# Performance work log

Measured on AMD Instinct MI355X. Metric: run time of the kernel, lower is better.

The kernel has to match this reference:

```python
import jax, jax.numpy as jnp
import numpy as np

EMBED_DIM = 768
NUM_HEADS = 12
HEAD_DIM = EMBED_DIM // NUM_HEADS
MLP_HIDDEN = int(EMBED_DIM * 4.0)
LN_EPS = 1e-5


def setup_inputs() -> dict:
    key = jax.random.key(0)
    ks = jax.random.split(key, 8)
    C, H = EMBED_DIM, MLP_HIDDEN
    s = 0.02
    return {
        "x": jax.random.normal(ks[0], (2, 2048, C), dtype=jnp.float32),
        "ln1_g": jnp.ones((C,), jnp.float32),
        "ln1_b": jnp.zeros((C,), jnp.float32),
        "qkv_w": jax.random.normal(ks[1], (3 * C, C), jnp.float32) * s,
        "proj_w": jax.random.normal(ks[2], (C, C), jnp.float32) * s,
        "proj_b": jnp.zeros((C,), jnp.float32),
        "ln2_g": jnp.ones((C,), jnp.float32),
        "ln2_b": jnp.zeros((C,), jnp.float32),
        "fc1_w": jax.random.normal(ks[3], (H, C), jnp.float32) * s,
        "fc1_b": jnp.zeros((H,), jnp.float32),
        "fc2_w": jax.random.normal(ks[4], (C, H), jnp.float32) * s,
        "fc2_b": jnp.zeros((C,), jnp.float32),
    }


def _layernorm(x, g, b):
    mu = jnp.mean(x, axis=-1, keepdims=True)
    var = jnp.mean(jnp.square(x - mu), axis=-1, keepdims=True)
    return (x - mu) * jax.lax.rsqrt(var + LN_EPS) * g + b


def reference(x, ln1_g, ln1_b, qkv_w, proj_w, proj_b, ln2_g, ln2_b,
              fc1_w, fc1_b, fc2_w, fc2_b):
    B, N, C = x.shape
    Hh, Dh = NUM_HEADS, HEAD_DIM
    scale = Dh ** -0.5

    # --- attention branch (pre-norm) ---
    h = _layernorm(x, ln1_g, ln1_b)
    qkv = h @ qkv_w.T                                   # [B,N,3C]
    qkv = qkv.reshape(B, N, 3, Hh, Dh)
    q = qkv[:, :, 0].transpose(0, 2, 1, 3)              # [B,H,N,D]
    k = qkv[:, :, 1].transpose(0, 2, 1, 3)
    v = qkv[:, :, 2].transpose(0, 2, 1, 3)
    attn = jnp.einsum('bhnd,bhmd->bhnm', q, k) * scale  # [B,H,N,N]
    attn = jax.nn.softmax(attn, axis=-1)
    o = jnp.einsum('bhnm,bhmd->bhnd', attn, v)          # [B,H,N,D]
    o = o.transpose(0, 2, 1, 3).reshape(B, N, C)
    x = x + o @ proj_w.T + proj_b

    # --- MLP branch (pre-norm), exact GELU like nn.GELU ---
    h = _layernorm(x, ln2_g, ln2_b)
    h = jax.nn.gelu(h @ fc1_w.T + fc1_b, approximate=False)
    x = x + h @ fc2_w.T + fc2_b
    return x
```

## Files before the change

kernel.cpp:

```cpp
#include <hip/hip_runtime.h>
#include <hip/hip_bf16.h>
#include <cstdint>
#include <math.h>


typedef __bf16 bf16_t;
typedef bf16_t bf16x4 __attribute__((ext_vector_type(4)));
typedef bf16_t bf16x8 __attribute__((ext_vector_type(8)));
typedef float floatx4 __attribute__((ext_vector_type(4)));

#define AS1 __attribute__((address_space(1)))
#define AS3 __attribute__((address_space(3)))

__device__ __forceinline__ void async_load16(const void* g, void* l) {
  const AS1 unsigned int* gp =
      reinterpret_cast<const AS1 unsigned int*>(reinterpret_cast<uintptr_t>(g));
  AS3 unsigned int* lp = reinterpret_cast<AS3 unsigned int*>(
      static_cast<unsigned int>(reinterpret_cast<uintptr_t>(l)));
  __builtin_amdgcn_global_load_lds(gp, lp, 16, 0, 0);
}

__device__ __forceinline__ bf16x8 lds_read8(const bf16_t* p) {
  return *reinterpret_cast<const bf16x8*>(p);
}

__global__ __launch_bounds__(256) void cvt_k(const float* __restrict__ in,
                                             bf16_t* __restrict__ out, int n4) {
  const int i = blockIdx.x * 256 + threadIdx.x;
  if (i < n4) {
    const float4 v = reinterpret_cast<const float4*>(in)[i];
    bf16x4 o;
    o[0] = (bf16_t)v.x; o[1] = (bf16_t)v.y; o[2] = (bf16_t)v.z; o[3] = (bf16_t)v.w;
    reinterpret_cast<bf16x4*>(out)[i] = o;
  }
}

__global__ __launch_bounds__(256) void cvt_all_k(
    const float* __restrict__ s0, const float* __restrict__ s1,
    const float* __restrict__ s2, const float* __restrict__ s3,
    bf16_t* __restrict__ d0, bf16_t* __restrict__ d1, bf16_t* __restrict__ d2,
    bf16_t* __restrict__ d3) {
  int i = blockIdx.x * 256 + threadIdx.x;
  const float* src;
  bf16_t* dst;
  if (i < 442368) { src = s0; dst = d0; }
  else if (i < 589824) { src = s1; dst = d1; i -= 442368; }
  else if (i < 1179648) { src = s2; dst = d2; i -= 589824; }
  else if (i < 1769472) { src = s3; dst = d3; i -= 1179648; }
  else return;
  const float4 v = reinterpret_cast<const float4*>(src)[i];
  bf16x4 o;
  o[0] = (bf16_t)v.x; o[1] = (bf16_t)v.y; o[2] = (bf16_t)v.z; o[3] = (bf16_t)v.w;
  reinterpret_cast<bf16x4*>(dst)[i] = o;
}

template <int INIT>
__global__ __launch_bounds__(256) void ln_k(const float* __restrict__ x,
                                            const float* __restrict__ g,
                                            const float* __restrict__ b,
                                            bf16_t* __restrict__ out,
                                            const float* __restrict__ b2,
                                            float* __restrict__ oinit) {
  const int row = blockIdx.x;
  const int tid = threadIdx.x;
  const float* xr = x + (long)row * 768;
  float v[3];
#pragma unroll
  for (int e = 0; e < 3; e++) v[e] = xr[tid + e * 256];
  float s = v[0] + v[1] + v[2];
  float ss = v[0] * v[0] + v[1] * v[1] + v[2] * v[2];
#pragma unroll
  for (int off = 32; off >= 1; off >>= 1) {
    s += __shfl_down(s, off, 64);
    ss += __shfl_down(ss, off, 64);
  }
  __shared__ float red[8];
  __shared__ float stat[2];
  const int wv = tid >> 6;
  if ((tid & 63) == 0) { red[wv] = s; red[4 + wv] = ss; }
  __syncthreads();
  if (tid == 0) {
    float S = red[0] + red[1] + red[2] + red[3];
    float SS = red[4] + red[5] + red[6] + red[7];
    float mu = S * (1.0f / 768.0f);
    float var = SS * (1.0f / 768.0f) - mu * mu;
    stat[0] = mu;
    stat[1] = rsqrtf(var + 1e-5f);
  }
  __syncthreads();
  const float mu = stat[0], rs = stat[1];
#pragma unroll
  for (int e = 0; e < 3; e++) {
    int c = tid + e * 256;
    out[(long)row * 768 + c] = (bf16_t)((v[e] - mu) * rs * g[c] + b[c]);
    if constexpr (INIT == 1) oinit[(long)row * 768 + c] = v[e] + b2[c];
  }
}

template <int MODE>
__global__ __launch_bounds__(256, 2) void gemm_k(
    const bf16_t* __restrict__ A, const bf16_t* __restrict__ Bt, int lda,
    int ldb, int keff, int Nld, const float* __restrict__ bias,
    bf16_t* __restrict__ out_bf, bf16_t* __restrict__ q_out,
    bf16_t* __restrict__ k_out, bf16_t* __restrict__ vt_out,
    const float* __restrict__ resid_f, float* __restrict__ out_f) {
  constexpr int BK = 32;
  __shared__ __align__(16) bf16_t As[3][128 * BK];
  __shared__ __align__(16) bf16_t Bs[3][128 * BK];

  const int tid = threadIdx.x;
  const int w = tid >> 6;
  const int lane = tid & 63;
  const int quad = lane >> 4;
  const int lid = lane & 15;
  const int wr = (w >> 1) * 64;
  const int wc = (w & 1) * 64;
  const int mBase = blockIdx.x * 128;
  const int nBase = blockIdx.y * 128;
  const int kOff = blockIdx.z * keff;

  const int ldsRowSub = lane >> 2;
  const int kblk = (lane & 3) ^ (ldsRowSub & 3) ^ ((ldsRowSub >> 2) & 3);
  const int rq0 = (quad ^ (lid & 3) ^ ((lid >> 2) & 3)) * 8;
  const int c0 = w * 2, c1 = w * 2 + 1;
  const int rowA0 = c0 * 16 + ldsRowSub, rowA1 = c1 * 16 + ldsRowSub;

  const bf16_t* Ag = A + (long)mBase * lda + kOff;
  const bf16_t* Bg = Bt + (long)nBase * ldb + kOff;

  floatx4 acc[4][4];
#pragma unroll
  for (int i = 0; i < 4; i++)
#pragma unroll
    for (int j = 0; j < 4; j++) acc[i][j] = (floatx4){0.f, 0.f, 0.f, 0.f};

  auto stage = [&](int b, int k0) {
    async_load16(Ag + (long)rowA0 * lda + k0 + kblk * 8, &As[b][c0 * 512]);
    async_load16(Ag + (long)rowA1 * lda + k0 + kblk * 8, &As[b][c1 * 512]);
    async_load16(Bg + (long)rowA0 * ldb + k0 + kblk * 8, &Bs[b][c0 * 512]);
    async_load16(Bg + (long)rowA1 * ldb + k0 + kblk * 8, &Bs[b][c1 * 512]);
  };

  const int iters = keff / BK;
  stage(0, 0);
  stage(1, BK);

  int cur = 0;
  for (int it = 0; it < iters; it++) {
    if (it + 1 < iters)
      asm volatile("s_waitcnt vmcnt(4) lgkmcnt(0)" ::: "memory");
    else
      asm volatile("s_waitcnt vmcnt(0) lgkmcnt(0)" ::: "memory");
    __builtin_amdgcn_s_barrier();
    if (it + 2 < iters) {
      int nb = cur + 2; if (nb >= 3) nb -= 3;
      stage(nb, (it + 2) * BK);
    }

    bf16x8 af[4], bfv[4];
#pragma unroll
    for (int i = 0; i < 4; i++)
      af[i] = lds_read8(&As[cur][(wr + i * 16 + lid) * BK + rq0]);
#pragma unroll
    for (int j = 0; j < 4; j++)
      bfv[j] = lds_read8(&Bs[cur][(wc + j * 16 + lid) * BK + rq0]);
#pragma unroll
    for (int i = 0; i < 4; i++)
#pragma unroll
      for (int j = 0; j < 4; j++)
        acc[i][j] = __builtin_amdgcn_mfma_f32_16x16x32_bf16(af[i], bfv[j],
                                                            acc[i][j], 0, 0, 0);
    cur = (cur == 2) ? 0 : cur + 1;
  }

#pragma unroll
  for (int i = 0; i < 4; i++) {
    const int mRow = mBase + wr + i * 16 + quad * 4;
#pragma unroll
    for (int j = 0; j < 4; j++) {
      const int n = nBase + wc + j * 16 + lid;
      if constexpr (MODE == 0) {
        const int which = n / 768;
        const int rem = n - which * 768;
        const int head = rem >> 6;
        const int d = rem & 63;
        const int b = mRow >> 11;
        const int t = mRow & 2047;
        const int bh = b * 12 + head;
        if (which == 2) {
          bf16x4 pk;
#pragma unroll
          for (int r = 0; r < 4; r++) pk[r] = (bf16_t)acc[i][j][r];
          const long off = ((long)bh * 64 + d) * 2048 + t;
          *reinterpret_cast<bf16x4*>(&vt_out[off]) = pk;
        } else if (which == 0) {
#pragma unroll
          for (int r = 0; r < 4; r++)
            q_out[((long)bh * 2048 + t + r) * 64 + d] =
                (bf16_t)(acc[i][j][r] * (0.125f * 1.44269504f));
        } else {
#pragma unroll
          for (int r = 0; r < 4; r++)
            k_out[((long)bh * 2048 + t + r) * 64 + d] = (bf16_t)acc[i][j][r];
        }
      } else if constexpr (MODE == 2) {
        const float bv = bias[n];
#pragma unroll
        for (int r = 0; r < 4; r++) {
          float v = acc[i][j][r] + bv;
          float ge = 0.5f * v * (1.0f + erff(v * 0.70710678118654752f));
          out_bf[(long)(mRow + r) * Nld + n] = (bf16_t)ge;
        }
      } else if constexpr (MODE == 3) {
        const float bv = bias[n];
#pragma unroll
        for (int r = 0; r < 4; r++) {
          const long off = (long)(mRow + r) * Nld + n;
          out_f[off] = resid_f[off] + acc[i][j][r] + bv;
        }
      } else {
#pragma unroll
        for (int r = 0; r < 4; r++) {
          const long off = (long)(mRow + r) * Nld + n;
          unsafeAtomicAdd(&out_f[off], acc[i][j][r]);
        }
      }
    }
  }
}

__global__ __launch_bounds__(512, 1) void flash_k(const bf16_t* __restrict__ q,
                                                  const bf16_t* __restrict__ kk,
                                                  const bf16_t* __restrict__ vt,
                                                  bf16_t* __restrict__ U,
                                                  float* __restrict__ lbuf) {
  constexpr int SK = 64, D = 64;
  __shared__ __align__(16) bf16_t Ks[3][SK * D];
  __shared__ __align__(16) bf16_t Vs[3][D * SK];

  const int tid = threadIdx.x;
  const int w = tid >> 6;
  const int lane = tid & 63;
  const int quad = lane >> 4;
  const int lid = lane & 15;
  const int bh = blockIdx.y;
  const int half = blockIdx.z;
  const int qBase = blockIdx.x * 128;

  const bf16_t* qg = q + ((long)bh * 2048 + qBase) * D;
  const bf16_t* kg = kk + ((long)bh * 2048 + half * 1024) * D;
  const bf16_t* vg = vt + (long)bh * D * 2048 + half * 1024;

  bf16x8 aq[2];
#pragma unroll
  for (int k2 = 0; k2 < 2; k2++)
    aq[k2] = *reinterpret_cast<const bf16x8*>(qg + (w * 16 + lid) * D +
                                              k2 * 32 + quad * 8);

  const int srow = lane >> 3;
  const int sdb = (lane & 7) ^ srow;
  const int rsw = lid & 7;

  auto stagef = [&](int b, int kc) {
    async_load16(kg + (long)(kc + w * 8 + srow) * D + sdb * 8, &Ks[b][w * 512]);
    async_load16(vg + (long)(w * 8 + srow) * 2048 + kc + sdb * 8, &Vs[b][w * 512]);
  };

  stagef(0, 0);
  stagef(1, 64);

  float lsum = 0.f;
  floatx4 oacc[4];
#pragma unroll
  for (int jo = 0; jo < 4; jo++) oacc[jo] = (floatx4){0.f, 0.f, 0.f, 0.f};

  int cur = 0;
  for (int kci = 0; kci < 16; kci++) {
    if (kci + 1 < 16)
      asm volatile("s_waitcnt vmcnt(2) lgkmcnt(0)" ::: "memory");
    else
      asm volatile("s_waitcnt vmcnt(0) lgkmcnt(0)" ::: "memory");
    __builtin_amdgcn_s_barrier();
    if (kci + 2 < 16) {
      int nb = cur + 2; if (nb >= 3) nb -= 3;
      stagef(nb, (kci + 2) * 64);
    }

    floatx4 sacc[4];
#pragma unroll
    for (int jm = 0; jm < 4; jm++) sacc[jm] = (floatx4){0.f, 0.f, 0.f, 0.f};
    __builtin_amdgcn_s_setprio(1);
#pragma unroll
    for (int k2 = 0; k2 < 2; k2++) {
#pragma unroll
      for (int jm = 0; jm < 4; jm++) {
        const bf16x8 ak = lds_read8(
            &Ks[cur][(jm * 16 + lid) * D + (((k2 * 4 + quad) ^ rsw) * 8)]);
        sacc[jm] =
            __builtin_amdgcn_mfma_f32_16x16x32_bf16(ak, aq[k2], sacc[jm], 0, 0, 0);
      }
    }
    __builtin_amdgcn_s_setprio(0);

    bf16x8 ap[2];
#pragma unroll
    for (int k2 = 0; k2 < 2; k2++) {
      uint32_t pk[2][2];
#pragma unroll
      for (int j = 0; j < 2; j++) {
        const int jm = k2 * 2 + j;
        const float p0 = exp2f(sacc[jm][0]);
        const float p1 = exp2f(sacc[jm][1]);
        const float p2 = exp2f(sacc[jm][2]);
        const float p3 = exp2f(sacc[jm][3]);
        lsum += ((p0 + p1) + p2) + p3;
        asm("v_cvt_pk_bf16_f32 %0, %1, %2" : "=v"(pk[j][0]) : "v"(p0), "v"(p1));
        asm("v_cvt_pk_bf16_f32 %0, %1, %2" : "=v"(pk[j][1]) : "v"(p2), "v"(p3));
      }
      asm("v_permlane32_swap_b32 %0, %1" : "+v"(pk[0][0]), "+v"(pk[1][0]));
      asm("v_permlane16_swap_b32 %0, %1" : "+v"(pk[0][0]), "+v"(pk[1][0]));
      asm("v_permlane32_swap_b32 %0, %1" : "+v"(pk[0][1]), "+v"(pk[1][1]));
      asm("v_permlane16_swap_b32 %0, %1" : "+v"(pk[0][1]), "+v"(pk[1][1]));
      union { uint32_t u[4]; bf16x8 v; } au;
      au.u[0] = pk[0][0];
      au.u[1] = pk[0][1];
      au.u[2] = pk[1][0];
      au.u[3] = pk[1][1];
      ap[k2] = au.v;
    }

    __builtin_amdgcn_s_setprio(1);
#pragma unroll
    for (int k2 = 0; k2 < 2; k2++) {
#pragma unroll
      for (int jo = 0; jo < 4; jo++) {
        const bf16x8 bv = lds_read8(
            &Vs[cur][(jo * 16 + lid) * SK + (((k2 * 4 + quad) ^ rsw) * 8)]);
        oacc[jo] =
            __builtin_amdgcn_mfma_f32_16x16x32_bf16(ap[k2], bv, oacc[jo], 0, 0, 0);
      }
    }
    __builtin_amdgcn_s_setprio(0);
    cur = (cur == 2) ? 0 : cur + 1;
  }

  lsum += __shfl_xor(lsum, 16, 64);
  lsum += __shfl_xor(lsum, 32, 64);

  const long lrow = ((long)half * 24 + bh) * 2048 + qBase + w * 16;
  if (quad == 0) lbuf[lrow + lid] = lsum;

  bf16_t* Ub = U + (((long)half * 24 + bh) * 2048 + qBase) * D;
#pragma unroll
  for (int jo = 0; jo < 4; jo++) {
#pragma unroll
    for (int r = 0; r < 4; r++) {
      const int t = w * 16 + quad * 4 + r;
      Ub[(long)t * D + jo * 16 + lid] = (bf16_t)oacc[jo][r];
    }
  }
}

__global__ __launch_bounds__(256) void combine_k(const bf16_t* __restrict__ U,
                                                 const float* __restrict__ lbuf,
                                                 bf16_t* __restrict__ o) {
  const int idx = blockIdx.x * 256 + threadIdx.x;
  const int bh = idx >> 17;
  const int rem = idx & 131071;
  const int t = rem >> 6;
  const int d = rem & 63;
  const float l0 = lbuf[bh * 2048 + t];
  const float l1 = lbuf[(24 + bh) * 2048 + t];
  const float u = (float)U[idx] + (float)U[3145728 + idx];
  const int b = bh / 12;
  const int head = bh - b * 12;
  o[((long)b * 2048 + t) * 768 + head * 64 + d] = (bf16_t)(u / (l0 + l1));
}

extern "C" void kernel_launch(void* const* d_in, const int* in_sizes, int n_in,
                              void* d_out, int out_size, void* d_ws,
                              size_t ws_size, hipStream_t stream) {
  (void)in_sizes; (void)n_in; (void)out_size;
  const float* x = (const float*)d_in[0];
  const float* ln1_g = (const float*)d_in[1];
  const float* ln1_b = (const float*)d_in[2];
  const float* qkv_w = (const float*)d_in[3];
  const float* proj_w = (const float*)d_in[4];
  const float* proj_b = (const float*)d_in[5];
  const float* ln2_g = (const float*)d_in[6];
  const float* ln2_b = (const float*)d_in[7];
  const float* fc1_w = (const float*)d_in[8];
  const float* fc1_b = (const float*)d_in[9];
  const float* fc2_w = (const float*)d_in[10];
  const float* fc2_b = (const float*)d_in[11];
  float* out = (float*)d_out;
  char* ws = (char*)d_ws;

  const bool big = ws_size >= (size_t)64487424;

  if (big) {
    bf16_t* wqkv = (bf16_t*)(ws + 0);
    bf16_t* wproj = (bf16_t*)(ws + 3538944);
    bf16_t* wfc1 = (bf16_t*)(ws + 4718592);
    bf16_t* wfc2 = (bf16_t*)(ws + 9437184);
    bf16_t* h1 = (bf16_t*)(ws + 14155776);
    bf16_t* ob = h1;
    bf16_t* qb = (bf16_t*)(ws + 20447232);
    bf16_t* kb = (bf16_t*)(ws + 26738688);
    bf16_t* vtb = (bf16_t*)(ws + 33030144);
    bf16_t* Ubuf = (bf16_t*)(ws + 39321600);
    float* lbuf = (float*)(ws + 51904512);
    float* x1 = (float*)(ws + 20447232);
    bf16_t* h2 = (bf16_t*)(ws + 33030144);
    bf16_t* hg = (bf16_t*)(ws + 39321600);

    cvt_all_k<<<6912, 256, 0, stream>>>(qkv_w, proj_w, fc1_w, fc2_w, wqkv,
                                        wproj, wfc1, wfc2);
    ln_k<0><<<4096, 256, 0, stream>>>(x, ln1_g, ln1_b, h1, nullptr, nullptr);
    gemm_k<0><<<dim3(32, 18), 256, 0, stream>>>(h1, wqkv, 768, 768, 768, 2304,
                                                nullptr, nullptr, qb, kb, vtb,
                                                nullptr, nullptr);
    flash_k<<<dim3(16, 24, 2), 512, 0, stream>>>(qb, kb, vtb, Ubuf, lbuf);
    combine_k<<<12288, 256, 0, stream>>>(Ubuf, lbuf, ob);
    gemm_k<3><<<dim3(32, 6), 256, 0, stream>>>(ob, wproj, 768, 768, 768, 768,
                                               proj_b, nullptr, nullptr,
                                               nullptr, nullptr, x, x1);
    ln_k<1><<<4096, 256, 0, stream>>>(x1, ln2_g, ln2_b, h2, fc2_b, out);
    gemm_k<2><<<dim3(32, 24), 256, 0, stream>>>(h2, wfc1, 768, 768, 768, 3072,
                                                fc1_b, hg, nullptr, nullptr,
                                                nullptr, nullptr, nullptr);
    gemm_k<4><<<dim3(32, 6, 2), 256, 0, stream>>>(hg, wfc2, 3072, 3072, 1536,
                                                  768, nullptr, nullptr,
                                                  nullptr, nullptr, nullptr,
                                                  nullptr, out);
  } else {
    bf16_t* wqkv = (bf16_t*)(ws + 0);
    bf16_t* wproj = (bf16_t*)(ws + 3538944);
    bf16_t* h1 = (bf16_t*)(ws + 4718592);
    bf16_t* ob = h1;
    bf16_t* qb = (bf16_t*)(ws + 11010048);
    bf16_t* kb = (bf16_t*)(ws + 17301504);
    bf16_t* vtb = (bf16_t*)(ws + 23592960);
    float* x1 = (float*)(ws + 11010048);
    bf16_t* h2 = (bf16_t*)(ws + 23592960);
    bf16_t* wfc1 = (bf16_t*)(ws + 0);
    bf16_t* wfc2 = (bf16_t*)(ws + 4718592);
    bf16_t* hg = (bf16_t*)(ws + 29884416);
    bf16_t* Ubuf = (bf16_t*)(ws + 29884416);
    float* lbuf = (float*)(ws + 42467328);

    cvt_k<<<1728, 256, 0, stream>>>(qkv_w, wqkv, 442368);
    cvt_k<<<576, 256, 0, stream>>>(proj_w, wproj, 147456);
    ln_k<0><<<4096, 256, 0, stream>>>(x, ln1_g, ln1_b, h1, nullptr, nullptr);
    gemm_k<0><<<dim3(32, 18), 256, 0, stream>>>(h1, wqkv, 768, 768, 768, 2304,
                                                nullptr, nullptr, qb, kb, vtb,
                                                nullptr, nullptr);
    flash_k<<<dim3(16, 24, 2), 512, 0, stream>>>(qb, kb, vtb, Ubuf, lbuf);
    combine_k<<<12288, 256, 0, stream>>>(Ubuf, lbuf, ob);
    gemm_k<3><<<dim3(32, 6), 256, 0, stream>>>(ob, wproj, 768, 768, 768, 768,
                                               proj_b, nullptr, nullptr,
                                               nullptr, nullptr, x, x1);
    cvt_k<<<2304, 256, 0, stream>>>(fc1_w, wfc1, 589824);
    cvt_k<<<2304, 256, 0, stream>>>(fc2_w, wfc2, 589824);
    ln_k<1><<<4096, 256, 0, stream>>>(x1, ln2_g, ln2_b, h2, fc2_b, out);
    for (int h = 0; h < 2; h++) {
      gemm_k<2><<<dim3(32, 12), 256, 0, stream>>>(
          h2, wfc1 + (long)h * 1536 * 768, 768, 768, 768, 1536,
          fc1_b + h * 1536, hg, nullptr, nullptr, nullptr, nullptr, nullptr);
      gemm_k<4><<<dim3(32, 6), 256, 0, stream>>>(hg, wfc2 + h * 1536, 1536,
                                                 3072, 1536, 768, nullptr,
                                                 nullptr, nullptr, nullptr,
                                                 nullptr, nullptr, out);
    }
  }
}
```

Baseline: 281.3 us.

## Load K/V directly from global memory in flash kernel, drop LDS staging

Measured after the change: 429.8 us. 1.53x slower.

```diff
diff --git a/kernel.cpp b/kernel.cpp
--- a/kernel.cpp
+++ b/kernel.cpp
@@ -229,61 +229,47 @@
   }
 }
 
-__global__ __launch_bounds__(512, 1) void flash_k(const bf16_t* __restrict__ q,
+__global__ __launch_bounds__(256, 3) void flash_k(const bf16_t* __restrict__ q,
                                                   const bf16_t* __restrict__ kk,
                                                   const bf16_t* __restrict__ vt,
                                                   bf16_t* __restrict__ U,
                                                   float* __restrict__ lbuf) {
-  constexpr int SK = 64, D = 64;
-  __shared__ __align__(16) bf16_t Ks[3][SK * D];
-  __shared__ __align__(16) bf16_t Vs[3][D * SK];
-
   const int tid = threadIdx.x;
   const int w = tid >> 6;
   const int lane = tid & 63;
   const int quad = lane >> 4;
   const int lid = lane & 15;
-  const int bh = blockIdx.y;
+  const int bh = blockIdx.x;
+  const int qBase = blockIdx.y * 64;
   const int half = blockIdx.z;
-  const int qBase = blockIdx.x * 128;
-
-  const bf16_t* qg = q + ((long)bh * 2048 + qBase) * D;
-  const bf16_t* kg = kk + ((long)bh * 2048 + half * 1024) * D;
-  const bf16_t* vg = vt + (long)bh * D * 2048 + half * 1024;
+
+  const bf16_t* qg = q + ((long)bh * 2048 + qBase) * 64;
+  const bf16_t* kg = kk + ((long)bh * 2048 + half * 1024) * 64;
+  const bf16_t* vg = vt + (long)bh * 64 * 2048 + half * 1024;
 
   bf16x8 aq[2];
 #pragma unroll
   for (int k2 = 0; k2 < 2; k2++)
-    aq[k2] = *reinterpret_cast<const bf16x8*>(qg + (w * 16 + lid) * D +
+    aq[k2] = *reinterpret_cast<const bf16x8*>(qg + (w * 16 + lid) * 64 +
                                               k2 * 32 + quad * 8);
 
-  const int srow = lane >> 3;
-  const int sdb = (lane & 7) ^ srow;
-  const int rsw = lid & 7;
-
-  auto stagef = [&](int b, int kc) {
-    async_load16(kg + (long)(kc + w * 8 + srow) * D + sdb * 8, &Ks[b][w * 512]);
-    async_load16(vg + (long)(w * 8 + srow) * 2048 + kc + sdb * 8, &Vs[b][w * 512]);
-  };
-
-  stagef(0, 0);
-  stagef(1, 64);
+  const bf16_t* kl = kg + lid * 64 + quad * 8;
+  const bf16_t* vl = vg + (long)lid * 2048 + quad * 8;
 
   float lsum = 0.f;
   floatx4 oacc[4];
 #pragma unroll
   for (int jo = 0; jo < 4; jo++) oacc[jo] = (floatx4){0.f, 0.f, 0.f, 0.f};
 
-  int cur = 0;
   for (int kci = 0; kci < 16; kci++) {
-    if (kci + 1 < 16)
-      asm volatile("s_waitcnt vmcnt(2) lgkmcnt(0)" ::: "memory");
-    else
-      asm volatile("s_waitcnt vmcnt(0) lgkmcnt(0)" ::: "memory");
-    __builtin_amdgcn_s_barrier();
-    if (kci + 2 < 16) {
-      int nb = cur + 2; if (nb >= 3) nb -= 3;
-      stagef(nb, (kci + 2) * 64);
+    const int kc = kci * 64;
+
+    bf16x8 ak0[4], ak1[4];
+#pragma unroll
+    for (int jm = 0; jm < 4; jm++) {
+      const bf16_t* kr = kl + (long)(kc + jm * 16) * 64;
+      ak0[jm] = *reinterpret_cast<const bf16x8*>(kr);
+      ak1[jm] = *reinterpret_cast<const bf16x8*>(kr + 32);
     }
 
     floatx4 sacc[4];
@@ -291,16 +277,22 @@
     for (int jm = 0; jm < 4; jm++) sacc[jm] = (floatx4){0.f, 0.f, 0.f, 0.f};
     __builtin_amdgcn_s_setprio(1);
 #pragma unroll
-    for (int k2 = 0; k2 < 2; k2++) {
-#pragma unroll
-      for (int jm = 0; jm < 4; jm++) {
-        const bf16x8 ak = lds_read8(
-            &Ks[cur][(jm * 16 + lid) * D + (((k2 * 4 + quad) ^ rsw) * 8)]);
-        sacc[jm] =
-            __builtin_amdgcn_mfma_f32_16x16x32_bf16(ak, aq[k2], sacc[jm], 0, 0, 0);
-      }
-    }
+    for (int jm = 0; jm < 4; jm++)
+      sacc[jm] = __builtin_amdgcn_mfma_f32_16x16x32_bf16(ak0[jm], aq[0],
+                                                         sacc[jm], 0, 0, 0);
+#pragma unroll
+    for (int jm = 0; jm < 4; jm++)
+      sacc[jm] = __builtin_amdgcn_mfma_f32_16x16x32_bf16(ak1[jm], aq[1],
+                                                         sacc[jm], 0, 0, 0);
     __builtin_amdgcn_s_setprio(0);
+
+    bf16x8 bv0[4], bv1[4];
+#pragma unroll
+    for (int jo = 0; jo < 4; jo++) {
+      const bf16_t* vr = vl + (long)jo * 16 * 2048 + kc;
+      bv0[jo] = *reinterpret_cast<const bf16x8*>(vr);
+      bv1[jo] = *reinterpret_cast<const bf16x8*>(vr + 32);
+    }
 
     bf16x8 ap[2];
 #pragma unroll
@@ -331,17 +323,14 @@
 
     __builtin_amdgcn_s_setprio(1);
 #pragma unroll
-    for (int k2 = 0; k2 < 2; k2++) {
-#pragma unroll
-      for (int jo = 0; jo < 4; jo++) {
-        const bf16x8 bv = lds_read8(
-            &Vs[cur][(jo * 16 + lid) * SK + (((k2 * 4 + quad) ^ rsw) * 8)]);
-        oacc[jo] =
-            __builtin_amdgcn_mfma_f32_16x16x32_bf16(ap[k2], bv, oacc[jo], 0, 0, 0);
-      }
-    }
+    for (int jo = 0; jo < 4; jo++)
+      oacc[jo] = __builtin_amdgcn_mfma_f32_16x16x32_bf16(ap[0], bv0[jo],
+                                                         oacc[jo], 0, 0, 0);
+#pragma unroll
+    for (int jo = 0; jo < 4; jo++)
+      oacc[jo] = __builtin_amdgcn_mfma_f32_16x16x32_bf16(ap[1], bv1[jo],
+                                                         oacc[jo], 0, 0, 0);
     __builtin_amdgcn_s_setprio(0);
-    cur = (cur == 2) ? 0 : cur + 1;
   }
 
   lsum += __shfl_xor(lsum, 16, 64);
@@ -350,13 +339,13 @@
   const long lrow = ((long)half * 24 + bh) * 2048 + qBase + w * 16;
   if (quad == 0) lbuf[lrow + lid] = lsum;
 
-  bf16_t* Ub = U + (((long)half * 24 + bh) * 2048 + qBase) * D;
+  bf16_t* Ub = U + (((long)half * 24 + bh) * 2048 + qBase) * 64;
 #pragma unroll
   for (int jo = 0; jo < 4; jo++) {
 #pragma unroll
     for (int r = 0; r < 4; r++) {
       const int t = w * 16 + quad * 4 + r;
-      Ub[(long)t * D + jo * 16 + lid] = (bf16_t)oacc[jo][r];
+      Ub[(long)t * 64 + jo * 16 + lid] = (bf16_t)oacc[jo][r];
     }
   }
 }
@@ -420,7 +409,7 @@
     gemm_k<0><<<dim3(32, 18), 256, 0, stream>>>(h1, wqkv, 768, 768, 768, 2304,
                                                 nullptr, nullptr, qb, kb, vtb,
                                                 nullptr, nullptr);
-    flash_k<<<dim3(16, 24, 2), 512, 0, stream>>>(qb, kb, vtb, Ubuf, lbuf);
+    flash_k<<<dim3(24, 32, 2), 256, 0, stream>>>(qb, kb, vtb, Ubuf, lbuf);
     combine_k<<<12288, 256, 0, stream>>>(Ubuf, lbuf, ob);
     gemm_k<3><<<dim3(32, 6), 256, 0, stream>>>(ob, wproj, 768, 768, 768, 768,
                                                proj_b, nullptr, nullptr,
@@ -455,7 +444,7 @@
     gemm_k<0><<<dim3(32, 18), 256, 0, stream>>>(h1, wqkv, 768, 768, 768, 2304,
                                                 nullptr, nullptr, qb, kb, vtb,
                                                 nullptr, nullptr);
-    flash_k<<<dim3(16, 24, 2), 512, 0, stream>>>(qb, kb, vtb, Ubuf, lbuf);
+    flash_k<<<dim3(24, 32, 2), 256, 0, stream>>>(qb, kb, vtb, Ubuf, lbuf);
     combine_k<<<12288, 256, 0, stream>>>(Ubuf, lbuf, ob);
     gemm_k<3><<<dim3(32, 6), 256, 0, stream>>>(ob, wproj, 768, 768, 768, 768,
                                                proj_b, nullptr, nullptr,
```
